# Kernel optimization log

Measured on AMD Instinct MI355X. Metric: run time of the kernel, lower is better.

The kernel has to match this reference:

```python
import jax, jax.numpy as jnp
import numpy as np

NEG_BIG = -9e15  # matches torch's -9000000000000000.0 mask value


def _gat_layer(x, adj_mask, W, a):
    # x: [N, Fin], W: [Fin, Fout], a: [Fout]
    h = x @ W                                   # [N, Fout]
    d = jnp.abs(h[None, :, :] - h[:, None, :])  # [N, N, Fout] pairwise |h_j - h_i|
    e = jax.nn.relu(jnp.einsum('ijf,f->ij', d, a))
    e = jnp.where(adj_mask, e, NEG_BIG)
    att = jax.nn.softmax(e, axis=1)             # row softmax (dropout p=0, skipped)
    return jax.nn.relu(att @ h)


def setup_inputs() -> dict:
    key = jax.random.key(0)
    ks = jax.random.split(key, 10)
    N, F, H, C = 1024, 128, 128, 16

    def xavier(k, shape, gain=1.414):
        fan_in, fan_out = shape[0], shape[-1]
        bound = gain * np.sqrt(6.0 / (fan_in + fan_out))
        return jax.random.uniform(k, shape, jnp.float32, -bound, bound)

    feat = jax.random.normal(ks[0], (N, F), jnp.float32)
    adj = jax.random.randint(ks[1], (N, N), 0, 2, jnp.int32)
    return {
        'feat': feat,
        'adj': adj,
        'W1': xavier(ks[2], (F, H)), 'a1': xavier(ks[3], (H, 1)).squeeze(-1),
        'W2': xavier(ks[4], (H, H)), 'a2': xavier(ks[5], (H, 1)).squeeze(-1),
        'W3': xavier(ks[6], (H, H)), 'a3': xavier(ks[7], (H, 1)).squeeze(-1),
        'Wfc': xavier(ks[8], (H, C), gain=1.0),
        'bfc': jnp.zeros((C,), jnp.float32),
    }


def reference(feat, adj, W1, a1, W2, a2, W3, a3, Wfc, bfc):
    mask = adj > 0
    x = _gat_layer(feat, mask, W1, a1)
    x = _gat_layer(x, mask, W2, a2)
    x = _gat_layer(x, mask, W3, a3)
    # EdgeGCN (include_adj=False): pairwise abs-diff -> linear, output [N*N, C]
    N, H = x.shape
    diff = jnp.abs(x[None, :, :] - x[:, None, :]).reshape(N * N, H)
    return diff @ Wfc + bfc
```

## Files before the change

### kernel.cpp

```cpp
#include <hip/hip_runtime.h>
#include <math.h>

#define NEG_BIG -9.0e15f

typedef __attribute__((ext_vector_type(4))) float f32x4;
typedef __attribute__((ext_vector_type(8))) short bf16x8;
typedef __attribute__((ext_vector_type(4))) unsigned int u32x4;

__global__ __launch_bounds__(128) void gemm_xw_t(const float* __restrict__ X,
                                                 const float* __restrict__ W,
                                                 float* __restrict__ HT) {
  __shared__ float xrow[128];
  const int i = blockIdx.x;
  const int o = threadIdx.x;
  xrow[o] = X[(size_t)i * 128 + o];
  __syncthreads();
  float acc = 0.f;
#pragma unroll 16
  for (int k = 0; k < 128; ++k) acc = fmaf(xrow[k], W[(size_t)k * 128 + o], acc);
  HT[(size_t)o * 1024 + i] = acc;
}

#define DOT4(acc, hv, p) \
  acc = fmaf(hv.x, p.x, fmaf(hv.y, p.y, fmaf(hv.z, p.z, fmaf(hv.w, p.w, acc))));

#define ABSFMA4R(accR, hv, hs, av)                  \
  accR.x = fmaf(fabsf(hv.x - hs), av, accR.x);      \
  accR.y = fmaf(fabsf(hv.y - hs), av, accR.y);      \
  accR.z = fmaf(fabsf(hv.z - hs), av, accR.z);      \
  accR.w = fmaf(fabsf(hv.w - hs), av, accR.w);

__global__ __launch_bounds__(1024, 4) void gat_attn(const float* __restrict__ HT,
                                                    const int* __restrict__ adj,
                                                    const float* __restrict__ a,
                                                    float* __restrict__ Xout) {
  __shared__ float4 ep4[4][4][256];
  __shared__ float e_s[4][1024];
  __shared__ float4 h4_s[128];
  __shared__ float a_s[128];
  __shared__ float redm[4][4];
  __shared__ float redsum[4][4];
  __shared__ float inv_s[4];

  const int t = threadIdx.x;
  const int i0 = blockIdx.x * 4;
  const float4* __restrict__ HT4 = reinterpret_cast<const float4*>(HT);

  if (t < 128) {
    h4_s[t] = *reinterpret_cast<const float4*>(HT + ((size_t)t << 10) + i0);
    a_s[t] = a[t];
  }
  __syncthreads();

  const int fq = t >> 8;
  const int jt = t & 255;
  const int il = t >> 8;
  const int j0 = jt * 4;

  float4 ac0 = {0.f, 0.f, 0.f, 0.f};
  float4 ac1 = {0.f, 0.f, 0.f, 0.f};
  float4 ac2 = {0.f, 0.f, 0.f, 0.f};
  float4 ac3 = {0.f, 0.f, 0.f, 0.f};
#pragma unroll 8
  for (int ff = 0; ff < 32; ++ff) {
    const int f = fq * 32 + ff;
    const float4 hv = HT4[f * 256 + jt];
    const float4 h4 = h4_s[f];
    const float av = a_s[f];
    ABSFMA4R(ac0, hv, h4.x, av);
    ABSFMA4R(ac1, hv, h4.y, av);
    ABSFMA4R(ac2, hv, h4.z, av);
    ABSFMA4R(ac3, hv, h4.w, av);
  }
  ep4[fq][0][jt] = ac0;
  ep4[fq][1][jt] = ac1;
  ep4[fq][2][jt] = ac2;
  ep4[fq][3][jt] = ac3;
  __syncthreads();

  float4 esum;
  {
    const float4 s0 = ep4[0][il][jt];
    const float4 s1 = ep4[1][il][jt];
    const float4 s2 = ep4[2][il][jt];
    const float4 s3 = ep4[3][il][jt];
    esum.x = (s0.x + s1.x) + (s2.x + s3.x);
    esum.y = (s0.y + s1.y) + (s2.y + s3.y);
    esum.z = (s0.z + s1.z) + (s2.z + s3.z);
    esum.w = (s0.w + s1.w) + (s2.w + s3.w);
  }

  float4 e;
  {
    const int4 ad = *reinterpret_cast<const int4*>(&adj[(size_t)(i0 + il) * 1024 + j0]);
    e.x = ad.x > 0 ? fmaxf(esum.x, 0.f) : NEG_BIG;
    e.y = ad.y > 0 ? fmaxf(esum.y, 0.f) : NEG_BIG;
    e.z = ad.z > 0 ? fmaxf(esum.z, 0.f) : NEG_BIG;
    e.w = ad.w > 0 ? fmaxf(esum.w, 0.f) : NEG_BIG;
  }

  const int wq = (t >> 6) & 3;
  float m = fmaxf(fmaxf(e.x, e.y), fmaxf(e.z, e.w));
#pragma unroll
  for (int off = 32; off > 0; off >>= 1) m = fmaxf(m, __shfl_xor(m, off));
  if ((t & 63) == 0) redm[il][wq] = m;
  __syncthreads();
  m = fmaxf(fmaxf(redm[il][0], redm[il][1]), fmaxf(redm[il][2], redm[il][3]));
  float4 p;
  p.x = __expf(e.x - m);
  p.y = __expf(e.y - m);
  p.z = __expf(e.z - m);
  p.w = __expf(e.w - m);
  *reinterpret_cast<float4*>(&e_s[il][j0]) = p;
  float s = p.x + p.y + p.z + p.w;
#pragma unroll
  for (int off = 32; off > 0; off >>= 1) s += __shfl_xor(s, off);
  if ((t & 63) == 0) redsum[il][wq] = s;
  __syncthreads();
  if (t < 4) {
    const float ss = redsum[t][0] + redsum[t][1] + redsum[t][2] + redsum[t][3];
    inv_s[t] = 1.f / ss;
  }
  __syncthreads();

  const int w = t >> 6;
  const int l = t & 63;
  const int f0 = w * 8;
  float acc[8][4];
#pragma unroll
  for (int ff = 0; ff < 8; ++ff)
#pragma unroll
    for (int r = 0; r < 4; ++r) acc[ff][r] = 0.f;

#pragma unroll
  for (int jb = 0; jb < 4; ++jb) {
    const int j4 = jb * 64 + l;
    const float4 p0 = *reinterpret_cast<const float4*>(&e_s[0][j4 * 4]);
    const float4 p1 = *reinterpret_cast<const float4*>(&e_s[1][j4 * 4]);
    const float4 p2 = *reinterpret_cast<const float4*>(&e_s[2][j4 * 4]);
    const float4 p3 = *reinterpret_cast<const float4*>(&e_s[3][j4 * 4]);
#pragma unroll
    for (int ff = 0; ff < 8; ++ff) {
      const float4 hv = HT4[(f0 + ff) * 256 + j4];
      DOT4(acc[ff][0], hv, p0);
      DOT4(acc[ff][1], hv, p1);
      DOT4(acc[ff][2], hv, p2);
      DOT4(acc[ff][3], hv, p3);
    }
  }

  float v[32];
#pragma unroll
  for (int ff = 0; ff < 8; ++ff)
#pragma unroll
    for (int r = 0; r < 4; ++r) v[ff * 4 + r] = acc[ff][r];

#pragma unroll
  for (int step = 0; step < 5; ++step) {
    const int s2 = 1 << step;
    const bool hi = (l & s2) != 0;
#pragma unroll
    for (int k = 0; k < (32 >> (step + 1)); ++k) {
      const float x = v[2 * k];
      const float y = v[2 * k + 1];
      float tt = hi ? x : y;
      tt = __shfl_xor(tt, s2);
      v[k] = (hi ? y : x) + tt;
    }
  }
  float r = v[0] + __shfl_xor(v[0], 32);

  if (l < 32) {
    const int oidx = l & 31;
    const int ff = oidx >> 2;
    const int orow = oidx & 3;
    const float o = fmaxf(r * inv_s[orow], 0.f);
    Xout[(size_t)(i0 + orow) * 128 + f0 + ff] = o;
  }
}

__global__ __launch_bounds__(256) void edge_fc_mfma(const float* __restrict__ X,
                                                    const float* __restrict__ Wfc,
                                                    const float* __restrict__ bfc,
                                                    float* __restrict__ out) {
  __shared__ float xi_s[32][132];
  __shared__ float xj_s[32][132];

  const int t = threadIdx.x;
  const int ib = blockIdx.x >> 5;
  const int jb = blockIdx.x & 31;

  {
    const int r = t >> 3;
    const int c0 = (t & 7) * 16;
    const float4* gi = reinterpret_cast<const float4*>(X + (size_t)(ib * 32 + r) * 128 + c0);
    const float4* gj = reinterpret_cast<const float4*>(X + (size_t)(jb * 32 + r) * 128 + c0);
#pragma unroll
    for (int k = 0; k < 4; ++k) {
      *reinterpret_cast<float4*>(&xi_s[r][c0 + k * 4]) = gi[k];
      *reinterpret_cast<float4*>(&xj_s[r][c0 + k * 4]) = gj[k];
    }
  }

  const int w = t >> 6, lane = t & 63;
  const int col = lane & 15, kg = lane >> 4;

  bf16x8 bhi[4], blo[4];
#pragma unroll
  for (int c = 0; c < 4; ++c) {
    bf16x8 bh, bl;
#pragma unroll
    for (int j = 0; j < 8; ++j) {
      const float wv = Wfc[(c * 32 + kg * 8 + j) * 16 + col];
      const unsigned u = __builtin_bit_cast(unsigned, wv);
      const unsigned h = u & 0xffff0000u;
      const float lof = wv - __builtin_bit_cast(float, h);
      bh[j] = (short)(h >> 16);
      bl[j] = (short)(__builtin_bit_cast(unsigned, lof) >> 16);
    }
    bhi[c] = bh;
    blo[c] = bl;
  }
  const float bb = bfc[col];

  __syncthreads();

  unsigned xjr[2][4][8];
#pragma unroll
  for (int jt = 0; jt < 2; ++jt) {
#pragma unroll
    for (int c = 0; c < 4; ++c) {
      const float4 v0 = *reinterpret_cast<const float4*>(&xj_s[jt * 16 + col][c * 32 + kg * 8]);
      const float4 v1 = *reinterpret_cast<const float4*>(&xj_s[jt * 16 + col][c * 32 + kg * 8 + 4]);
      xjr[jt][c][0] = __builtin_bit_cast(unsigned, v0.x);
      xjr[jt][c][1] = __builtin_bit_cast(unsigned, v0.y);
      xjr[jt][c][2] = __builtin_bit_cast(unsigned, v0.z);
      xjr[jt][c][3] = __builtin_bit_cast(unsigned, v0.w);
      xjr[jt][c][4] = __builtin_bit_cast(unsigned, v1.x);
      xjr[jt][c][5] = __builtin_bit_cast(unsigned, v1.y);
      xjr[jt][c][6] = __builtin_bit_cast(unsigned, v1.z);
      xjr[jt][c][7] = __builtin_bit_cast(unsigned, v1.w);
    }
  }

  const int iq = w;

  for (int i = 0; i < 8; ++i) {
    const int li = iq * 8 + i;
    const int gi = ib * 32 + li;
    f32x4 acc0 = {bb, bb, bb, bb};
    f32x4 acc1 = {bb, bb, bb, bb};
#pragma unroll
    for (int c = 0; c < 4; ++c) {
      const float4 v0 = *reinterpret_cast<const float4*>(&xi_s[li][c * 32 + kg * 8]);
      const float4 v1 = *reinterpret_cast<const float4*>(&xi_s[li][c * 32 + kg * 8 + 4]);
      unsigned xiv[8];
      xiv[0] = __builtin_bit_cast(unsigned, v0.x);
      xiv[1] = __builtin_bit_cast(unsigned, v0.y);
      xiv[2] = __builtin_bit_cast(unsigned, v0.z);
      xiv[3] = __builtin_bit_cast(unsigned, v0.w);
      xiv[4] = __builtin_bit_cast(unsigned, v1.x);
      xiv[5] = __builtin_bit_cast(unsigned, v1.y);
      xiv[6] = __builtin_bit_cast(unsigned, v1.z);
      xiv[7] = __builtin_bit_cast(unsigned, v1.w);
#pragma unroll
      for (int jt = 0; jt < 2; ++jt) {
        u32x4 ahv, alv;
#pragma unroll
        for (int q = 0; q < 4; ++q) {
          const float d0 = __builtin_bit_cast(float, xjr[jt][c][2 * q]) -
                           __builtin_bit_cast(float, xiv[2 * q]);
          const float d1 = __builtin_bit_cast(float, xjr[jt][c][2 * q + 1]) -
                           __builtin_bit_cast(float, xiv[2 * q + 1]);
          const unsigned h0 = __builtin_bit_cast(unsigned, d0) & 0x7fff0000u;
          const unsigned h1 = __builtin_bit_cast(unsigned, d1) & 0x7fff0000u;
          const float lo0 = fabsf(d0) - __builtin_bit_cast(float, h0);
          const float lo1 = fabsf(d1) - __builtin_bit_cast(float, h1);
          ahv[q] = __builtin_amdgcn_perm(h1, h0, 0x07060302u);
          alv[q] = __builtin_amdgcn_perm(__builtin_bit_cast(unsigned, lo1),
                                         __builtin_bit_cast(unsigned, lo0), 0x07060302u);
        }
        const bf16x8 ah = __builtin_bit_cast(bf16x8, ahv);
        const bf16x8 al = __builtin_bit_cast(bf16x8, alv);
        if (jt == 0) {
          acc0 = __builtin_amdgcn_mfma_f32_16x16x32_bf16(ah, bhi[c], acc0, 0, 0, 0);
          acc0 = __builtin_amdgcn_mfma_f32_16x16x32_bf16(ah, blo[c], acc0, 0, 0, 0);
          acc0 = __builtin_amdgcn_mfma_f32_16x16x32_bf16(al, bhi[c], acc0, 0, 0, 0);
        } else {
          acc1 = __builtin_amdgcn_mfma_f32_16x16x32_bf16(ah, bhi[c], acc1, 0, 0, 0);
          acc1 = __builtin_amdgcn_mfma_f32_16x16x32_bf16(ah, blo[c], acc1, 0, 0, 0);
          acc1 = __builtin_amdgcn_mfma_f32_16x16x32_bf16(al, bhi[c], acc1, 0, 0, 0);
        }
      }
    }
    const size_t obase = (size_t)gi * 1024;
#pragma unroll
    for (int r = 0; r < 4; ++r) {
      const int gj0 = jb * 32 + kg * 4 + r;
      const int gj1 = gj0 + 16;
      __builtin_nontemporal_store(acc0[r], out + (obase + gj0) * 16 + col);
      __builtin_nontemporal_store(acc1[r], out + (obase + gj1) * 16 + col);
    }
  }
}

extern "C" void kernel_launch(void* const* d_in, const int* in_sizes, int n_in,
                              void* d_out, int out_size, void* d_ws, size_t ws_size,
                              hipStream_t stream) {
  const float* feat = (const float*)d_in[0];
  const int* adj = (const int*)d_in[1];
  const float* W1 = (const float*)d_in[2];
  const float* a1 = (const float*)d_in[3];
  const float* W2 = (const float*)d_in[4];
  const float* a2 = (const float*)d_in[5];
  const float* W3 = (const float*)d_in[6];
  const float* a3 = (const float*)d_in[7];
  const float* Wfc = (const float*)d_in[8];
  const float* bfc = (const float*)d_in[9];
  float* out = (float*)d_out;

  float* ht = (float*)d_ws;
  float* xA = ht + 131072;
  float* xB = xA + 131072;

  gemm_xw_t<<<1024, 128, 0, stream>>>(feat, W1, ht);
  gat_attn<<<256, 1024, 0, stream>>>(ht, adj, a1, xA);
  gemm_xw_t<<<1024, 128, 0, stream>>>(xA, W2, ht);
  gat_attn<<<256, 1024, 0, stream>>>(ht, adj, a2, xB);
  gemm_xw_t<<<1024, 128, 0, stream>>>(xB, W3, ht);
  gat_attn<<<256, 1024, 0, stream>>>(ht, adj, a3, xA);
  edge_fc_mfma<<<1024, 256, 0, stream>>>(xA, Wfc, bfc, out);
}
```

Baseline: 102.4 us.

## Process two rows per GAT attention block and double the grid

```diff
diff --git a/kernel.cpp b/kernel.cpp
--- a/kernel.cpp
+++ b/kernel.cpp
@@ -30,137 +30,129 @@
   accR.z = fmaf(fabsf(hv.z - hs), av, accR.z);      \
   accR.w = fmaf(fabsf(hv.w - hs), av, accR.w);
 
-__global__ __launch_bounds__(1024, 4) void gat_attn(const float* __restrict__ HT,
+__global__ __launch_bounds__(1024, 8) void gat_attn(const float* __restrict__ HT,
                                                     const int* __restrict__ adj,
                                                     const float* __restrict__ a,
                                                     float* __restrict__ Xout) {
-  __shared__ float4 ep4[4][4][256];
-  __shared__ float e_s[4][1024];
-  __shared__ float4 h4_s[128];
+  __shared__ float4 ep4[4][2][256];
+  __shared__ float e_s[2][1024];
+  __shared__ float2 h2_s[128];
   __shared__ float a_s[128];
-  __shared__ float redm[4][4];
-  __shared__ float redsum[4][4];
-  __shared__ float inv_s[4];
+  __shared__ float redm[2][8];
+  __shared__ float redsum[2][8];
+  __shared__ float inv_s[2];
 
   const int t = threadIdx.x;
-  const int i0 = blockIdx.x * 4;
+  const int i0 = blockIdx.x * 2;
   const float4* __restrict__ HT4 = reinterpret_cast<const float4*>(HT);
 
   if (t < 128) {
-    h4_s[t] = *reinterpret_cast<const float4*>(HT + ((size_t)t << 10) + i0);
+    h2_s[t] = *reinterpret_cast<const float2*>(HT + ((size_t)t << 10) + i0);
     a_s[t] = a[t];
   }
   __syncthreads();
 
   const int fq = t >> 8;
   const int jt = t & 255;
-  const int il = t >> 8;
-  const int j0 = jt * 4;
 
   float4 ac0 = {0.f, 0.f, 0.f, 0.f};
   float4 ac1 = {0.f, 0.f, 0.f, 0.f};
-  float4 ac2 = {0.f, 0.f, 0.f, 0.f};
-  float4 ac3 = {0.f, 0.f, 0.f, 0.f};
 #pragma unroll 8
   for (int ff = 0; ff < 32; ++ff) {
     const int f = fq * 32 + ff;
     const float4 hv = HT4[f * 256 + jt];
-    const float4 h4 = h4_s[f];
+    const float2 h2 = h2_s[f];
     const float av = a_s[f];
-    ABSFMA4R(ac0, hv, h4.x, av);
-    ABSFMA4R(ac1, hv, h4.y, av);
-    ABSFMA4R(ac2, hv, h4.z, av);
-    ABSFMA4R(ac3, hv, h4.w, av);
+    ABSFMA4R(ac0, hv, h2.x, av);
+    ABSFMA4R(ac1, hv, h2.y, av);
   }
   ep4[fq][0][jt] = ac0;
   ep4[fq][1][jt] = ac1;
-  ep4[fq][2][jt] = ac2;
-  ep4[fq][3][jt] = ac3;
-  __syncthreads();
-
-  float4 esum;
+  __syncthreads();
+
+  const int row = t >> 9;
+  const int jh = t & 511;
+  float2 esum;
   {
-    const float4 s0 = ep4[0][il][jt];
-    const float4 s1 = ep4[1][il][jt];
-    const float4 s2 = ep4[2][il][jt];
-    const float4 s3 = ep4[3][il][jt];
+    const float2* p0 = reinterpret_cast<const float2*>(&ep4[0][row][0]);
+    const float2* p1 = reinterpret_cast<const float2*>(&ep4[1][row][0]);
+    const float2* p2 = reinterpret_cast<const float2*>(&ep4[2][row][0]);
+    const float2* p3 = reinterpret_cast<const float2*>(&ep4[3][row][0]);
+    const float2 s0 = p0[jh], s1 = p1[jh], s2 = p2[jh], s3 = p3[jh];
     esum.x = (s0.x + s1.x) + (s2.x + s3.x);
     esum.y = (s0.y + s1.y) + (s2.y + s3.y);
-    esum.z = (s0.z + s1.z) + (s2.z + s3.z);
-    esum.w = (s0.w + s1.w) + (s2.w + s3.w);
-  }
-
-  float4 e;
+  }
+
+  float2 e;
   {
-    const int4 ad = *reinterpret_cast<const int4*>(&adj[(size_t)(i0 + il) * 1024 + j0]);
+    const int2 ad = *reinterpret_cast<const int2*>(&adj[(size_t)(i0 + row) * 1024 + jh * 2]);
     e.x = ad.x > 0 ? fmaxf(esum.x, 0.f) : NEG_BIG;
     e.y = ad.y > 0 ? fmaxf(esum.y, 0.f) : NEG_BIG;
-    e.z = ad.z > 0 ? fmaxf(esum.z, 0.f) : NEG_BIG;
-    e.w = ad.w > 0 ? fmaxf(esum.w, 0.f) : NEG_BIG;
-  }
-
-  const int wq = (t >> 6) & 3;
-  float m = fmaxf(fmaxf(e.x, e.y), fmaxf(e.z, e.w));
+  }
+
+  const int wq = (t >> 6) & 7;
+  float m = fmaxf(e.x, e.y);
 #pragma unroll
   for (int off = 32; off > 0; off >>= 1) m = fmaxf(m, __shfl_xor(m, off));
-  if ((t & 63) == 0) redm[il][wq] = m;
-  __syncthreads();
-  m = fmaxf(fmaxf(redm[il][0], redm[il][1]), fmaxf(redm[il][2], redm[il][3]));
-  float4 p;
+  if ((t & 63) == 0) redm[row][wq] = m;
+  __syncthreads();
+  {
+    const float4 m0 = *reinterpret_cast<const float4*>(&redm[row][0]);
+    const float4 m1 = *reinterpret_cast<const float4*>(&redm[row][4]);
+    m = fmaxf(fmaxf(fmaxf(m0.x, m0.y), fmaxf(m0.z, m0.w)),
+              fmaxf(fmaxf(m1.x, m1.y), fmaxf(m1.z, m1.w)));
+  }
+  float2 p;
   p.x = __expf(e.x - m);
   p.y = __expf(e.y - m);
-  p.z = __expf(e.z - m);
-  p.w = __expf(e.w - m);
-  *reinterpret_cast<float4*>(&e_s[il][j0]) = p;
-  float s = p.x + p.y + p.z + p.w;
+  *reinterpret_cast<float2*>(&e_s[row][jh * 2]) = p;
+  float s = p.x + p.y;
 #pragma unroll
   for (int off = 32; off > 0; off >>= 1) s += __shfl_xor(s, off);
-  if ((t & 63) == 0) redsum[il][wq] = s;
-  __syncthreads();
-  if (t < 4) {
-    const float ss = redsum[t][0] + redsum[t][1] + redsum[t][2] + redsum[t][3];
-    inv_s[t] = 1.f / ss;
+  if ((t & 63) == 0) redsum[row][wq] = s;
+  __syncthreads();
+  if (t < 2) {
+    const float4 s0 = *reinterpret_cast<const float4*>(&redsum[t][0]);
+    const float4 s1 = *reinterpret_cast<const float4*>(&redsum[t][4]);
+    inv_s[t] = 1.f / (s0.x + s0.y + s0.z + s0.w + s1.x + s1.y + s1.z + s1.w);
   }
   __syncthreads();
 
   const int w = t >> 6;
   const int l = t & 63;
   const int f0 = w * 8;
-  float acc[8][4];
-#pragma unroll
-  for (int ff = 0; ff < 8; ++ff)
-#pragma unroll
-    for (int r = 0; r < 4; ++r) acc[ff][r] = 0.f;
+  float acc[8][2];
+#pragma unroll
+  for (int ff = 0; ff < 8; ++ff) {
+    acc[ff][0] = 0.f;
+    acc[ff][1] = 0.f;
+  }
 
 #pragma unroll
   for (int jb = 0; jb < 4; ++jb) {
     const int j4 = jb * 64 + l;
     const float4 p0 = *reinterpret_cast<const float4*>(&e_s[0][j4 * 4]);
     const float4 p1 = *reinterpret_cast<const float4*>(&e_s[1][j4 * 4]);
-    const float4 p2 = *reinterpret_cast<const float4*>(&e_s[2][j4 * 4]);
-    const float4 p3 = *reinterpret_cast<const float4*>(&e_s[3][j4 * 4]);
 #pragma unroll
     for (int ff = 0; ff < 8; ++ff) {
       const float4 hv = HT4[(f0 + ff) * 256 + j4];
       DOT4(acc[ff][0], hv, p0);
       DOT4(acc[ff][1], hv, p1);
-      DOT4(acc[ff][2], hv, p2);
-      DOT4(acc[ff][3], hv, p3);
-    }
-  }
-
-  float v[32];
-#pragma unroll
-  for (int ff = 0; ff < 8; ++ff)
-#pragma unroll
-    for (int r = 0; r < 4; ++r) v[ff * 4 + r] = acc[ff][r];
-
-#pragma unroll
-  for (int step = 0; step < 5; ++step) {
+    }
+  }
+
+  float v[16];
+#pragma unroll
+  for (int ff = 0; ff < 8; ++ff) {
+    v[ff * 2 + 0] = acc[ff][0];
+    v[ff * 2 + 1] = acc[ff][1];
+  }
+#pragma unroll
+  for (int step = 0; step < 4; ++step) {
     const int s2 = 1 << step;
     const bool hi = (l & s2) != 0;
 #pragma unroll
-    for (int k = 0; k < (32 >> (step + 1)); ++k) {
+    for (int k = 0; k < (16 >> (step + 1)); ++k) {
       const float x = v[2 * k];
       const float y = v[2 * k + 1];
       float tt = hi ? x : y;
@@ -168,14 +160,14 @@
       v[k] = (hi ? y : x) + tt;
     }
   }
-  float r = v[0] + __shfl_xor(v[0], 32);
-
-  if (l < 32) {
-    const int oidx = l & 31;
-    const int ff = oidx >> 2;
-    const int orow = oidx & 3;
-    const float o = fmaxf(r * inv_s[orow], 0.f);
-    Xout[(size_t)(i0 + orow) * 128 + f0 + ff] = o;
+  float r0 = v[0];
+  r0 += __shfl_xor(r0, 16);
+  r0 += __shfl_xor(r0, 32);
+
+  if (l < 16) {
+    const int ff = l >> 1;
+    const int orow = l & 1;
+    Xout[(size_t)(i0 + orow) * 128 + f0 + ff] = fmaxf(r0 * inv_s[orow], 0.f);
   }
 }
 
@@ -324,10 +316,10 @@
   float* xB = xA + 131072;
 
   gemm_xw_t<<<1024, 128, 0, stream>>>(feat, W1, ht);
-  gat_attn<<<256, 1024, 0, stream>>>(ht, adj, a1, xA);
+  gat_attn<<<512, 1024, 0, stream>>>(ht, adj, a1, xA);
   gemm_xw_t<<<1024, 128, 0, stream>>>(xA, W2, ht);
-  gat_attn<<<256, 1024, 0, stream>>>(ht, adj, a2, xB);
+  gat_attn<<<512, 1024, 0, stream>>>(ht, adj, a2, xB);
   gemm_xw_t<<<1024, 128, 0, stream>>>(xB, W3, ht);
-  gat_attn<<<256, 1024, 0, stream>>>(ht, adj, a3, xA);
+  gat_attn<<<512, 1024, 0, stream>>>(ht, adj, a3, xA);
   edge_fc_mfma<<<1024, 256, 0, stream>>>(xA, Wfc, bfc, out);
 }
```

Result: slower. 126.7 us (+23.7%).

## Split GAT attention into score kernel and split-bf16 MFMA P·V kernel

Applied to the files above, without the earlier changes.

```diff
diff --git a/kernel.cpp b/kernel.cpp
--- a/kernel.cpp
+++ b/kernel.cpp
@@ -21,21 +21,34 @@
   HT[(size_t)o * 1024 + i] = acc;
 }
 
-#define DOT4(acc, hv, p) \
-  acc = fmaf(hv.x, p.x, fmaf(hv.y, p.y, fmaf(hv.z, p.z, fmaf(hv.w, p.w, acc))));
-
 #define ABSFMA4R(accR, hv, hs, av)                  \
   accR.x = fmaf(fabsf(hv.x - hs), av, accR.x);      \
   accR.y = fmaf(fabsf(hv.y - hs), av, accR.y);      \
   accR.z = fmaf(fabsf(hv.z - hs), av, accR.z);      \
   accR.w = fmaf(fabsf(hv.w - hs), av, accR.w);
 
-__global__ __launch_bounds__(1024, 4) void gat_attn(const float* __restrict__ HT,
-                                                    const int* __restrict__ adj,
-                                                    const float* __restrict__ a,
-                                                    float* __restrict__ Xout) {
+#define SPLIT8(srcArr, hiV, loV)                                               \
+  {                                                                            \
+    u32x4 hh, ll;                                                              \
+    _Pragma("unroll") for (int q = 0; q < 4; ++q) {                            \
+      const float v0f = srcArr[2 * q], v1f = srcArr[2 * q + 1];                \
+      const unsigned u0 = __builtin_bit_cast(unsigned, v0f) & 0xffff0000u;     \
+      const unsigned u1 = __builtin_bit_cast(unsigned, v1f) & 0xffff0000u;     \
+      const float l0 = v0f - __builtin_bit_cast(float, u0);                    \
+      const float l1 = v1f - __builtin_bit_cast(float, u1);                    \
+      hh[q] = __builtin_amdgcn_perm(u1, u0, 0x07060302u);                      \
+      ll[q] = __builtin_amdgcn_perm(__builtin_bit_cast(unsigned, l1),          \
+                                    __builtin_bit_cast(unsigned, l0), 0x07060302u); \
+    }                                                                          \
+    hiV = __builtin_bit_cast(bf16x8, hh);                                      \
+    loV = __builtin_bit_cast(bf16x8, ll);                                      \
+  }
+
+__global__ __launch_bounds__(1024, 4) void gat_escore(const float* __restrict__ HT,
+                                                      const int* __restrict__ adj,
+                                                      const float* __restrict__ a,
+                                                      float* __restrict__ P) {
   __shared__ float4 ep4[4][4][256];
-  __shared__ float e_s[4][1024];
   __shared__ float4 h4_s[128];
   __shared__ float a_s[128];
   __shared__ float redm[4][4];
@@ -111,7 +124,6 @@
   p.y = __expf(e.y - m);
   p.z = __expf(e.z - m);
   p.w = __expf(e.w - m);
-  *reinterpret_cast<float4*>(&e_s[il][j0]) = p;
   float s = p.x + p.y + p.z + p.w;
 #pragma unroll
   for (int off = 32; off > 0; off >>= 1) s += __shfl_xor(s, off);
@@ -123,59 +135,90 @@
   }
   __syncthreads();
 
-  const int w = t >> 6;
-  const int l = t & 63;
-  const int f0 = w * 8;
-  float acc[8][4];
-#pragma unroll
-  for (int ff = 0; ff < 8; ++ff)
-#pragma unroll
-    for (int r = 0; r < 4; ++r) acc[ff][r] = 0.f;
-
-#pragma unroll
-  for (int jb = 0; jb < 4; ++jb) {
-    const int j4 = jb * 64 + l;
-    const float4 p0 = *reinterpret_cast<const float4*>(&e_s[0][j4 * 4]);
-    const float4 p1 = *reinterpret_cast<const float4*>(&e_s[1][j4 * 4]);
-    const float4 p2 = *reinterpret_cast<const float4*>(&e_s[2][j4 * 4]);
-    const float4 p3 = *reinterpret_cast<const float4*>(&e_s[3][j4 * 4]);
-#pragma unroll
-    for (int ff = 0; ff < 8; ++ff) {
-      const float4 hv = HT4[(f0 + ff) * 256 + j4];
-      DOT4(acc[ff][0], hv, p0);
-      DOT4(acc[ff][1], hv, p1);
-      DOT4(acc[ff][2], hv, p2);
-      DOT4(acc[ff][3], hv, p3);
-    }
-  }
-
-  float v[32];
-#pragma unroll
-  for (int ff = 0; ff < 8; ++ff)
-#pragma unroll
-    for (int r = 0; r < 4; ++r) v[ff * 4 + r] = acc[ff][r];
-
-#pragma unroll
-  for (int step = 0; step < 5; ++step) {
-    const int s2 = 1 << step;
-    const bool hi = (l & s2) != 0;
-#pragma unroll
-    for (int k = 0; k < (32 >> (step + 1)); ++k) {
-      const float x = v[2 * k];
-      const float y = v[2 * k + 1];
-      float tt = hi ? x : y;
-      tt = __shfl_xor(tt, s2);
-      v[k] = (hi ? y : x) + tt;
-    }
-  }
-  float r = v[0] + __shfl_xor(v[0], 32);
-
-  if (l < 32) {
-    const int oidx = l & 31;
-    const int ff = oidx >> 2;
-    const int orow = oidx & 3;
-    const float o = fmaxf(r * inv_s[orow], 0.f);
-    Xout[(size_t)(i0 + orow) * 128 + f0 + ff] = o;
+  const float inv = inv_s[il];
+  float4 po;
+  po.x = p.x * inv;
+  po.y = p.y * inv;
+  po.z = p.z * inv;
+  po.w = p.w * inv;
+  *reinterpret_cast<float4*>(&P[(size_t)(i0 + il) * 1024 + j0]) = po;
+}
+
+__global__ __launch_bounds__(256) void att_pv(const float* __restrict__ P,
+                                              const float* __restrict__ HT,
+                                              float* __restrict__ X) {
+  __shared__ float4 p_s4[2][16][32];
+  __shared__ float4 h_s4[2][32][32];
+  __shared__ float dsum[2][16][16];
+
+  const int t = threadIdx.x;
+  const int it = blockIdx.x >> 2;
+  const int ft = blockIdx.x & 3;
+  const int w = t >> 6, lane = t & 63;
+  const int col = lane & 15, kg = lane >> 4;
+  const int nt = w & 1, kh = w >> 1;
+
+  f32x4 aHH = {0.f, 0.f, 0.f, 0.f};
+  f32x4 aHL = {0.f, 0.f, 0.f, 0.f};
+  f32x4 aLH = {0.f, 0.f, 0.f, 0.f};
+
+  for (int ch = 0; ch < 4; ++ch) {
+    __syncthreads();
+#pragma unroll
+    for (int k = 0; k < 12; ++k) {
+      const int idx = t + k * 256;
+      const int row = idx >> 5;
+      const int c4 = idx & 31;
+      if (row < 32) {
+        const int khp = row >> 4, ir = row & 15;
+        p_s4[khp][ir][c4] = *reinterpret_cast<const float4*>(
+            &P[(size_t)(it * 16 + ir) * 1024 + khp * 512 + ch * 128 + c4 * 4]);
+      } else {
+        const int r2 = row - 32;
+        const int khh = r2 >> 5, fr = r2 & 31;
+        h_s4[khh][fr][c4] = *reinterpret_cast<const float4*>(
+            &HT[(size_t)(ft * 32 + fr) * 1024 + khh * 512 + ch * 128 + c4 * 4]);
+      }
+    }
+    __syncthreads();
+
+#pragma unroll
+    for (int k32 = 0; k32 < 4; ++k32) {
+      const int jc = k32 * 32 + kg * 8;
+      const float* pr = reinterpret_cast<const float*>(&p_s4[kh][col][0]);
+      const float* hr = reinterpret_cast<const float*>(&h_s4[kh][nt * 16 + col][0]);
+      float pa[8], hb[8];
+      {
+        const float4 v0 = *reinterpret_cast<const float4*>(&pr[jc]);
+        const float4 v1 = *reinterpret_cast<const float4*>(&pr[jc + 4]);
+        pa[0] = v0.x; pa[1] = v0.y; pa[2] = v0.z; pa[3] = v0.w;
+        pa[4] = v1.x; pa[5] = v1.y; pa[6] = v1.z; pa[7] = v1.w;
+        const float4 u0 = *reinterpret_cast<const float4*>(&hr[jc]);
+        const float4 u1 = *reinterpret_cast<const float4*>(&hr[jc + 4]);
+        hb[0] = u0.x; hb[1] = u0.y; hb[2] = u0.z; hb[3] = u0.w;
+        hb[4] = u1.x; hb[5] = u1.y; hb[6] = u1.z; hb[7] = u1.w;
+      }
+      bf16x8 ah, al, bh, bl;
+      SPLIT8(pa, ah, al);
+      SPLIT8(hb, bh, bl);
+      aHH = __builtin_amdgcn_mfma_f32_16x16x32_bf16(ah, bh, aHH, 0, 0, 0);
+      aHL = __builtin_amdgcn_mfma_f32_16x16x32_bf16(ah, bl, aHL, 0, 0, 0);
+      aLH = __builtin_amdgcn_mfma_f32_16x16x32_bf16(al, bh, aLH, 0, 0, 0);
+    }
+  }
+
+  f32x4 acc = (aHH + aHL) + aLH;
+  if (kh == 1) {
+#pragma unroll
+    for (int r = 0; r < 4; ++r) dsum[nt][kg * 4 + r][col] = acc[r];
+  }
+  __syncthreads();
+  if (kh == 0) {
+#pragma unroll
+    for (int r = 0; r < 4; ++r) {
+      const float v = fmaxf(acc[r] + dsum[nt][kg * 4 + r][col], 0.f);
+      X[(size_t)(it * 16 + kg * 4 + r) * 128 + ft * 32 + nt * 16 + col] = v;
+    }
   }
 }
 
@@ -322,12 +365,16 @@
   float* ht = (float*)d_ws;
   float* xA = ht + 131072;
   float* xB = xA + 131072;
+  float* P = out;
 
   gemm_xw_t<<<1024, 128, 0, stream>>>(feat, W1, ht);
-  gat_attn<<<256, 1024, 0, stream>>>(ht, adj, a1, xA);
+  gat_escore<<<256, 1024, 0, stream>>>(ht, adj, a1, P);
+  att_pv<<<256, 256, 0, stream>>>(P, ht, xA);
   gemm_xw_t<<<1024, 128, 0, stream>>>(xA, W2, ht);
-  gat_attn<<<256, 1024, 0, stream>>>(ht, adj, a2, xB);
+  gat_escore<<<256, 1024, 0, stream>>>(ht, adj, a2, P);
+  att_pv<<<256, 256, 0, stream>>>(P, ht, xB);
   gemm_xw_t<<<1024, 128, 0, stream>>>(xB, W3, ht);
-  gat_attn<<<256, 1024, 0, stream>>>(ht, adj, a3, xA);
+  gat_escore<<<256, 1024, 0, stream>>>(ht, adj, a3, P);
+  att_pv<<<256, 256, 0, stream>>>(P, ht, xA);
   edge_fc_mfma<<<1024, 256, 0, stream>>>(xA, Wfc, bfc, out);
 }
```

New measurement: 131.0 us. 1.28x slower.
